# Kernel optimization log

Hardware: AMD Instinct MI355X
Metric: run time of the kernel (lower is better)

The kernel has to match this reference:

```python
import jax, jax.numpy as jnp
import numpy as np

B, V, L = 128, 128000, 200


def setup_inputs() -> dict:
    key = jax.random.key(0)
    k1, k2, k3, k4, k5, k6, k7 = jax.random.split(key, 7)
    return {
        "logits": jax.random.normal(k1, (B, V), dtype=jnp.float32),
        "presence_penalties": jax.random.uniform(k2, (B,), dtype=jnp.float32, minval=0.0, maxval=2.0),
        "frequency_penalties": jax.random.uniform(k3, (B,), dtype=jnp.float32, minval=0.0, maxval=2.0),
        "temperatures": jax.random.uniform(k4, (B,), dtype=jnp.float32, minval=0.5, maxval=1.5),
        "top_ps": jax.random.uniform(k5, (B,), dtype=jnp.float32, minval=0.7, maxval=1.0),
        "output_tokens": jax.random.randint(k6, (B, L), 0, V),
        "top_ks": jax.random.randint(k7, (B,), 1, 1000),
    }


def reference(logits, presence_penalties, frequency_penalties, temperatures,
              top_ps, output_tokens, top_ks):
    b, v = logits.shape
    # --- penalties: batched bincount via scatter-add (matches _batched_bincount,
    # including counting the 0-padded history tokens, as the torch code does) ---
    rows = jnp.arange(b)[:, None]
    occ = jnp.zeros((b, v), dtype=logits.dtype).at[rows, output_tokens].add(1.0)
    logits = logits - occ * frequency_penalties[:, None] \
                    - (occ > 0).astype(logits.dtype) * presence_penalties[:, None]
    # --- temperature ---
    logits = logits / temperatures[:, None]
    # --- top-p / top-k filtering (sort descending, mask, unsort) ---
    idx = jnp.argsort(-logits, axis=-1)                       # [b, v] descending order
    logits_sort = jnp.take_along_axis(logits, idx, axis=-1)
    probs_sort = jax.nn.softmax(logits_sort, axis=-1)
    probs_cum = jnp.cumsum(probs_sort, axis=-1)
    top_p_mask = (probs_cum - probs_sort) > top_ps[:, None]
    top_k_mask = jnp.arange(v)[None, :] >= top_ks[:, None]
    logits_sort = jnp.where(top_p_mask | top_k_mask, -jnp.inf, logits_sort)
    inv = jnp.argsort(idx, axis=-1)
    logits = jnp.take_along_axis(logits_sort, inv, axis=-1)   # back to vocab order
    # --- probs / logprobs ---
    probs = jax.nn.softmax(logits, axis=-1)
    logprobs = jax.nn.log_softmax(logits, axis=-1)
    # --- multinomial sample via Gumbel-max (deterministic fixed key) ---
    g = jax.random.gumbel(jax.random.key(42), (b, v), dtype=logits.dtype)
    next_tokens = jnp.argmax(logprobs + g, axis=-1)
    return probs, logprobs, next_tokens
```

## Files before the change

### kernel.cpp

```cpp
#include <hip/hip_runtime.h>
#include <stdint.h>


#define B_ 128
#define V_ 128000
#define L_ 200
#define NPREP_ 4
#define PQ_ (V_ / NPREP_)
#define PQ4_ (PQ_ / 4)
#define NCHUNK_ 16
#define CHUNK_ (V_ / NCHUNK_)
#define CHUNK4_ (CHUNK_ / 4)
#define NBIN_ 8192
#define PCAP_ 2048
#define CCAP_ (NPREP_ * PCAP_)
#define TCAP_ 2048

#define OFF_CAND_ 32
#define OFF_TIDX_ 50000
#define OFF_TYV_ 51000
#define OFF_HCNT_ 65568
static_assert(OFF_CAND_ + NPREP_ * 2 * PCAP_ <= OFF_TIDX_, "layout");
static_assert(OFF_TIDX_ + NPREP_ * L_ <= OFF_TYV_, "layout");
static_assert(OFF_TYV_ + NPREP_ * L_ <= OFF_HCNT_, "layout");
static_assert(OFF_HCNT_ + NPREP_ * NBIN_ <= V_, "layout");
static_assert(816 + L_ < CHUNK_, "relay layout");

#define JAX_PARTITIONABLE 1

__device__ __forceinline__ uint32_t f2key(float f) {
  uint32_t u = __float_as_uint(f);
  return (u & 0x80000000u) ? ~u : (u | 0x80000000u);
}
__device__ __forceinline__ float key2f(uint32_t k) {
  uint32_t u = (k & 0x80000000u) ? (k ^ 0x80000000u) : ~k;
  return __uint_as_float(u);
}
__device__ __forceinline__ float binhi(uint32_t bin) {
  return key2f((bin << 19) | 0x7FFFFu);
}

__device__ __forceinline__ float adj_pen(float x, float cnt, float fp, float pp, float tt) {
#pragma clang fp contract(off)
  return ((x - cnt * fp) - pp) / tt;
}
__device__ __forceinline__ float adj_plain(float x, float tt) {
#pragma clang fp contract(off)
  return x / tt;
}
__device__ __forceinline__ float fsub(float a, float b) {
#pragma clang fp contract(off)
  return a - b;
}

__device__ __forceinline__ void tf_round(uint32_t &a, uint32_t &b, int r) {
  a += b;
  b = (b << r) | (b >> (32 - r));
  b ^= a;
}
__device__ __forceinline__ void threefry2x32(uint32_t x0, uint32_t x1, uint32_t &o0, uint32_t &o1) {
  const uint32_t k0 = 0u, k1 = 42u;
  const uint32_t k2 = k0 ^ k1 ^ 0x1BD11BDAu;
  x0 += k0; x1 += k1;
  tf_round(x0, x1, 13); tf_round(x0, x1, 15); tf_round(x0, x1, 26); tf_round(x0, x1, 6);
  x0 += k1; x1 += k2 + 1u;
  tf_round(x0, x1, 17); tf_round(x0, x1, 29); tf_round(x0, x1, 16); tf_round(x0, x1, 24);
  x0 += k2; x1 += k0 + 2u;
  tf_round(x0, x1, 13); tf_round(x0, x1, 15); tf_round(x0, x1, 26); tf_round(x0, x1, 6);
  x0 += k0; x1 += k1 + 3u;
  tf_round(x0, x1, 17); tf_round(x0, x1, 29); tf_round(x0, x1, 16); tf_round(x0, x1, 24);
  x0 += k1; x1 += k2 + 4u;
  tf_round(x0, x1, 13); tf_round(x0, x1, 15); tf_round(x0, x1, 26); tf_round(x0, x1, 6);
  x0 += k2; x1 += k0 + 5u;
  o0 = x0; o1 = x1;
}
__device__ __forceinline__ float gumbel_at(uint32_t j) {
  uint32_t o0, o1, bits;
#if JAX_PARTITIONABLE
  threefry2x32(0u, j, o0, o1);
  bits = o0 ^ o1;
#else
  const uint32_t half = (uint32_t)B_ * (uint32_t)V_ / 2u;
  if (j < half) { threefry2x32(j, j + half, o0, o1); bits = o0; }
  else          { threefry2x32(j - half, j, o0, o1); bits = o1; }
#endif
  float u = __uint_as_float((bits >> 9) | 0x3f800000u) - 1.0f;
  float r = (u == 0.0f) ? 1.17549435e-38f : u;
  return -logf(-logf(r));
}

__global__ void __launch_bounds__(1024) k_prep_v14(
    const float* __restrict__ logits, const float* __restrict__ pres,
    const float* __restrict__ freq, const float* __restrict__ temps,
    const int* __restrict__ toks, float* __restrict__ probs) {
  const int b = blockIdx.y, q = blockIdx.x, tid = threadIdx.x;
  __shared__ int stok[L_];
  __shared__ uint32_t lhist[NBIN_];
  __shared__ uint32_t lk[PCAP_];
  __shared__ uint32_t li[PCAP_];
  __shared__ uint32_t bmap[PQ_ / 32];
  __shared__ uint32_t ptok[L_];
  __shared__ uint32_t pyv[L_];
  __shared__ uint32_t s_lcnt, s_pcnt;
  if (tid < L_) stok[tid] = toks[b * L_ + tid];
  for (int i = tid; i < NBIN_; i += 1024) lhist[i] = 0u;
  if (tid < PQ_ / 32 - 0) {  bmap[tid < PQ_ / 32 ? tid : 0] = 0u; }
  if (tid == 0) { s_lcnt = 0u; s_pcnt = 0u; }
  const float tt = temps[b];
  const uint32_t kth = f2key(adj_plain(2.0f, tt));
  __syncthreads();
  const int base4 = q * PQ4_;
  const int lo = q * PQ_;
  const float4* src = (const float4*)(logits + (size_t)b * V_);
  for (int it = 0; it < 8; ++it) {
    const int i4 = it * 1024 + tid;
    if (i4 < PQ4_) {
      const float4 x = src[base4 + i4];
      const float vv[4] = {adj_plain(x.x, tt), adj_plain(x.y, tt),
                           adj_plain(x.z, tt), adj_plain(x.w, tt)};
      const int v0 = (base4 + i4) * 4;
#pragma unroll
      for (int p = 0; p < 4; ++p) {
        const uint32_t k = f2key(vv[p]);
        atomicAdd(&lhist[k >> 19], 1u);
        if (k >= kth) {
          const uint32_t slot = atomicAdd(&s_lcnt, 1u);
          if (slot < PCAP_) { lk[slot] = k; li[slot] = (uint32_t)(v0 + p); }
        }
      }
    }
  }
  __syncthreads();
  if (tid < L_) {
    const int t0 = stok[tid];
    if (t0 >= lo && t0 < lo + PQ_) {
      int cnt = 0; bool first = true;
      for (int i = 0; i < L_; ++i) {
        const int ti = stok[i];
        cnt += (ti == t0);
        if (i < tid && ti == t0) first = false;
      }
      if (first) {
        const float x = logits[(size_t)b * V_ + t0];
        const float y_old = adj_plain(x, tt);
        const float y_new = adj_pen(x, (float)cnt, freq[b], pres[b], tt);
        atomicSub(&lhist[f2key(y_old) >> 19], 1u);
        atomicAdd(&lhist[f2key(y_new) >> 19], 1u);
        const int off = t0 - lo;
        atomicOr(&bmap[off >> 5], 1u << (off & 31));
        const uint32_t slot = atomicAdd(&s_pcnt, 1u);
        if (slot < (uint32_t)L_) {
          ptok[slot] = (uint32_t)t0;
          pyv[slot] = __float_as_uint(y_new);
        }
      }
    }
  }
  __syncthreads();
  const uint32_t lcnt = s_lcnt < PCAP_ ? s_lcnt : PCAP_;
  for (uint32_t i = tid; i < lcnt; i += 1024) {
    const uint32_t idx = li[i];
    const int off = (int)idx - lo;
    if (bmap[off >> 5] & (1u << (off & 31))) {
      int cnt = 0;
      for (int j = 0; j < L_; ++j) cnt += (stok[j] == (int)idx);
      const float x = logits[(size_t)b * V_ + idx];
      lk[i] = f2key(adj_pen(x, (float)cnt, freq[b], pres[b], tt));
    }
  }
  __syncthreads();
  uint32_t* stats = (uint32_t*)(probs + (size_t)b * V_);
  const uint32_t pcnt = s_pcnt < (uint32_t)L_ ? s_pcnt : (uint32_t)L_;
  if (tid == 0) {
    stats[1 + q] = lcnt;
    stats[16 + q] = pcnt;
  }
  uint32_t* slice = stats + OFF_HCNT_ + q * NBIN_;
  for (int i = tid; i < NBIN_; i += 1024) slice[i] = lhist[i];
  uint32_t* seg = stats + OFF_CAND_ + q * 2 * PCAP_;
  for (uint32_t i = tid; i < lcnt; i += 1024) {
    seg[2 * i] = lk[i]; seg[2 * i + 1] = li[i];
  }
  uint32_t* tidx = stats + OFF_TIDX_ + q * L_;
  uint32_t* tyv = stats + OFF_TYV_ + q * L_;
  for (uint32_t i = tid; i < pcnt; i += 1024) {
    tidx[i] = ptok[i]; tyv[i] = pyv[i];
  }
}

__global__ void __launch_bounds__(1024) k_mid_v14(
    const int* __restrict__ topks, const float* __restrict__ topps,
    float* __restrict__ probs, float* __restrict__ tail) {
  const int b = blockIdx.x, tid = threadIdx.x;
  uint32_t* stats = (uint32_t*)(probs + (size_t)b * V_);
  __shared__ uint32_t hcnt[NBIN_];
  __shared__ uint32_t sk[CCAP_];
  __shared__ uint32_t si[CCAP_];
  __shared__ uint32_t tbi[L_];
  __shared__ uint32_t tby[L_];
  __shared__ uint32_t tlist[TCAP_];
  __shared__ uint32_t ccnt[256];
  __shared__ float cw[256];
  __shared__ float zcw[256];
  __shared__ uint32_t mb[256];
  __shared__ uint32_t lh[256];
  __shared__ float scm[256];
  __shared__ uint32_t scc[256];
  __shared__ uint32_t sS[256];
  __shared__ float rf[1024];
  __shared__ unsigned long long ru[1024];
  __shared__ uint32_t s_r, s_prefix, s_pmask, s_tieE, s_tiemax, s_tcnt, s_n;
  __shared__ int s_pick, s_pick2, s_found;
  __shared__ float s_m;
  if (tid == 0) { s_tiemax = 0x7FFFFFFFu; s_tcnt = 0u; }
  const uint32_t c0 = stats[1] < PCAP_ ? stats[1] : PCAP_;
  const uint32_t c1 = stats[2] < PCAP_ ? stats[2] : PCAP_;
  const uint32_t c2 = stats[3] < PCAP_ ? stats[3] : PCAP_;
  const uint32_t c3 = stats[4] < PCAP_ ? stats[4] : PCAP_;
  const uint32_t e1 = c0 + c1, e2 = c0 + c1 + c2;
  const uint32_t C = e2 + c3;
  for (uint32_t c = tid; c < C; c += 1024) {
    uint32_t qq, rr;
    if (c < c0)      { qq = 0; rr = c; }
    else if (c < e1) { qq = 1; rr = c - c0; }
    else if (c < e2) { qq = 2; rr = c - e1; }
    else             { qq = 3; rr = c - e2; }
    const uint2 e = ((const uint2*)(stats + OFF_CAND_ + qq * 2 * PCAP_))[rr];
    sk[c] = e.x; si[c] = e.y;
  }
  uint32_t pc[NPREP_];
#pragma unroll
  for (int qq = 0; qq < NPREP_; ++qq) {
    const uint32_t nq = stats[16 + qq];
    pc[qq] = nq < (uint32_t)L_ ? nq : (uint32_t)L_;
  }
  uint32_t tp = 0;
#pragma unroll
  for (int qq = 0; qq < NPREP_; ++qq) {
    const uint32_t* gi = stats + OFF_TIDX_ + qq * L_;
    const uint32_t* gy = stats + OFF_TYV_ + qq * L_;
    for (uint32_t i = tid; i < pc[qq]; i += 1024) {
      const uint32_t d = tp + i;
      if (d < (uint32_t)L_) { tbi[d] = gi[i]; tby[d] = gy[i]; }
    }
    tp += pc[qq];
  }
  const uint32_t T = tp < (uint32_t)L_ ? tp : (uint32_t)L_;
  const uint32_t* hs = stats + OFF_HCNT_;
  for (int i = tid; i < NBIN_; i += 1024)
    hcnt[i] = hs[i] + hs[NBIN_ + i] + hs[2 * NBIN_ + i] + hs[3 * NBIN_ + i];
  __syncthreads();
  if (tid < 256) {
    uint32_t sc = 0; float sw = 0.0f; uint32_t mymb = 0u;
    const int hi = (NBIN_ - 1) - 32 * tid;
    for (int i = 0; i < 32; ++i) {
      const int bin = hi - i;
      const uint32_t c = hcnt[bin];
      sc += c;
      if (c) {
        sw += (float)c * __expf(binhi((uint32_t)bin));
        if ((uint32_t)bin > mymb) mymb = (uint32_t)bin;
      }
    }
    ccnt[tid] = sc; cw[tid] = sw; zcw[tid] = sw; mb[tid] = mymb;
  }
  __syncthreads();
  for (int s = 128; s > 0; s >>= 1) {
    if (tid < s) {
      mb[tid] = mb[tid] > mb[tid + s] ? mb[tid] : mb[tid + s];
      zcw[tid] += zcw[tid + s];
    }
    __syncthreads();
  }
  if (tid == 0) s_m = binhi(mb[0]);
  const float Z = zcw[0];
  const float limit = topps[b] * Z;
  if (tid < 256) { scm[tid] = cw[tid]; scc[tid] = ccnt[tid]; }
  __syncthreads();
  for (int off = 1; off < 256; off <<= 1) {
    float a = 0.0f; uint32_t u = 0u;
    const bool act = (tid < 256 && tid >= off);
    if (act) { a = scm[tid - off]; u = scc[tid - off]; }
    __syncthreads();
    if (act) { scm[tid] += a; scc[tid] += u; }
    __syncthreads();
  }
  if (tid == 0) s_pick = 256;
  __syncthreads();
  if (tid < 256) {
    const float ecm = tid ? scm[tid - 1] : 0.0f;
    if (ecm + cw[tid] > limit) atomicMin(&s_pick, tid);
  }
  __syncthreads();
  if (tid == 0) {
    uint32_t np = (uint32_t)V_;
    const int k = s_pick;
    if (k < 256) {
      float cm = k ? scm[k - 1] : 0.0f;
      uint32_t cc = k ? scc[k - 1] : 0u;
      const int hh = (NBIN_ - 1) - 32 * k;
      for (int i = 0; i < 32; ++i) {
        const int bin = hh - i;
        const uint32_t c = hcnt[bin];
        float rm = 0.0f;
        if (c) rm = (float)c * __expf(binhi((uint32_t)bin));
        cc += c; cm += rm;
        if (cm > limit) { np = cc; break; }
      }
    }
    const uint32_t K = (uint32_t)topks[b];
    uint32_t n = K < np ? K : np;
    if (n < 1u) n = 1u;
    s_n = n;
  }
  __syncthreads();
  const uint32_t n = s_n;
  if (tid == 0) s_pick2 = 256;
  __syncthreads();
  if (tid < 256) {
    if (scc[tid] >= n) atomicMin(&s_pick2, tid);
  }
  __syncthreads();
  if (tid == 0) {
    const int k2 = s_pick2 < 256 ? s_pick2 : 255;
    uint32_t cc = k2 ? scc[k2 - 1] : 0u;
    uint32_t istar = 0, cab = 0;
    const int hh = (NBIN_ - 1) - 32 * k2;
    for (int i = 0; i < 32; ++i) {
      const int bin = hh - i;
      if (cc + hcnt[bin] >= n) { istar = (uint32_t)bin; cab = cc; break; }
      cc += hcnt[bin];
    }
    s_r = n - cab;
    s_prefix = istar << 19;
    s_pmask = 0xFFF80000u;
  }
  __syncthreads();
  const float m = s_m;
  const int shifts[3] = {11, 3, 0};
  const uint32_t widths[3] = {256u, 256u, 8u};
  for (int p = 0; p < 3; ++p) {
    const int sh = shifts[p];
    const uint32_t w = widths[p];
    for (uint32_t i = tid; i < w; i += 1024) lh[i] = 0u;
    __syncthreads();
    const uint32_t pr = s_prefix, pm = s_pmask;
    for (uint32_t c = tid; c < C; c += 1024) {
      const uint32_t k = sk[c];
      if ((k & pm) == pr) atomicAdd(&lh[(k >> sh) & (w - 1u)], 1u);
    }
    __syncthreads();
    if (tid < (int)w) sS[tid] = lh[tid];
    __syncthreads();
    for (uint32_t off = 1; off < w; off <<= 1) {
      uint32_t a = 0u;
      const bool act = (tid + off < w);
      if (act) a = sS[tid + off];
      __syncthreads();
      if (act) sS[tid] += a;
      __syncthreads();
    }
    if (tid == 0) s_found = -1;
    __syncthreads();
    const uint32_t rr = s_r;
    if (tid < (int)w) {
      const uint32_t Shere = sS[tid];
      const uint32_t Snext = (tid + 1 < (int)w) ? sS[tid + 1] : 0u;
      if (Shere >= rr && Snext < rr) s_found = tid;
    }
    __syncthreads();
    if (tid == 0) {
      int found = s_found;
      if (found < 0) { found = 0; s_r = 1u; }
      else {
        const uint32_t Snext = (found + 1 < (int)w) ? sS[found + 1] : 0u;
        s_r = rr - Snext;
      }
      s_prefix = s_prefix | ((uint32_t)found << sh);
      s_pmask = s_pmask | ((w - 1u) << sh);
      s_tieE = lh[found];
    }
    __syncthreads();
  }
  const uint32_t tkey = s_prefix;
  const uint32_t ekeep = s_r;
  const uint32_t E = s_tieE;
  __syncthreads();
  if (ekeep < E && E <= (uint32_t)TCAP_) {
    for (uint32_t c = tid; c < C; c += 1024) {
      if (sk[c] == tkey) {
        const uint32_t pos = atomicAdd(&s_tcnt, 1u);
        if (pos < (uint32_t)TCAP_) tlist[pos] = si[c];
      }
    }
    __syncthreads();
    const uint32_t tc = s_tcnt < (uint32_t)TCAP_ ? s_tcnt : (uint32_t)TCAP_;
    for (uint32_t i = tid; i < tc; i += 1024) {
      const uint32_t mine = tlist[i];
      uint32_t rank = 0;
      for (uint32_t j = 0; j < tc; ++j) rank += (tlist[j] < mine) ? 1u : 0u;
      if (rank == ekeep - 1u) s_tiemax = mine;
    }
    __syncthreads();
  }
  const uint32_t tiemax = s_tiemax;
  float zp = 0.0f;
  for (uint32_t c = tid; c < C; c += 1024) {
    const uint32_t k = sk[c];
    if (k > tkey || (k == tkey && si[c] <= tiemax)) zp += expf(fsub(key2f(k), m));
  }
  rf[tid] = zp;
  __syncthreads();
  for (int s = 512; s > 0; s >>= 1) { if (tid < s) rf[tid] += rf[tid + s]; __syncthreads(); }
  const float Zp = rf[0];
  const float logZp = logf(Zp);
  unsigned long long best = 0ull;
  for (uint32_t c = tid; c < C; c += 1024) {
    const uint32_t k = sk[c];
    const uint32_t idx = si[c];
    if (k > tkey || (k == tkey && idx <= tiemax)) {
      const float lp = fsub(fsub(key2f(k), m), logZp);
      const float g = gumbel_at((uint32_t)b * (uint32_t)V_ + idx);
      const float sv = lp + g;
      const unsigned long long pk =
          ((unsigned long long)f2key(sv) << 32) | (unsigned long long)(~idx);
      if (pk > best) best = pk;
    }
  }
  ru[tid] = best;
  __syncthreads();
  for (int s = 512; s > 0; s >>= 1) {
    if (tid < s) ru[tid] = ru[tid] > ru[tid + s] ? ru[tid] : ru[tid + s];
    __syncthreads();
  }
  if (tid == 0) {
    const uint32_t bi = ~((uint32_t)(ru[0] & 0xFFFFFFFFull));
    tail[b] = (float)bi;
  }
  __syncthreads();
  if (tid < NCHUNK_) {
    uint32_t* cp = (uint32_t*)(probs + (size_t)b * V_ + (size_t)tid * CHUNK_);
    cp[0] = __float_as_uint(m);
    cp[1] = tkey;
    cp[2] = tiemax;
    cp[3] = __float_as_uint(Zp);
    cp[4] = __float_as_uint(logZp);
    cp[5] = T;
  }
  for (uint32_t i = tid; i < T; i += 1024) {
    const uint32_t a = tbi[i], yv = tby[i];
#pragma unroll
    for (int cc = 0; cc < NCHUNK_; ++cc) {
      uint32_t* cp = (uint32_t*)(probs + (size_t)b * V_ + (size_t)cc * CHUNK_);
      cp[16 + i] = a;
      cp[816 + i] = yv;
    }
  }
}

__global__ void __launch_bounds__(256) k_final_v14(
    const float* __restrict__ logits, const float* __restrict__ temps,
    float* __restrict__ probs, float* __restrict__ Ylp) {
  const int b = blockIdx.y, c = blockIdx.x, tid = threadIdx.x;
  float* cp = probs + (size_t)b * V_ + (size_t)c * CHUNK_;
  const uint32_t* cpu = (const uint32_t*)cp;
  __shared__ uint32_t sstat[6];
  __shared__ uint32_t tbi[L_], tby[L_];
  if (tid < 6) sstat[tid] = cpu[tid];
  __syncthreads();
  const uint32_t T = sstat[5] < (uint32_t)L_ ? sstat[5] : (uint32_t)L_;
  for (uint32_t i = tid; i < T; i += 256) { tbi[i] = cpu[16 + i]; tby[i] = cpu[816 + i]; }
  __syncthreads();
  const float m = __uint_as_float(sstat[0]);
  const uint32_t tkey = sstat[1];
  const uint32_t tiemax = sstat[2];
  const float Zp = __uint_as_float(sstat[3]);
  const float logZp = __uint_as_float(sstat[4]);
  const float tt = temps[b];
  const float nbig = -1e38f;
  const float4* xsrc = (const float4*)(logits + (size_t)b * V_ + (size_t)c * CHUNK_);
  float4* pdst = (float4*)cp;
  float4* ldst = (float4*)(Ylp + (size_t)b * V_ + (size_t)c * CHUNK_);
  for (int it = 0; it < 8; ++it) {
    const int i4 = it * 256 + tid;
    if (i4 < CHUNK4_) {
      const float4 x = xsrc[i4];
      const int v0 = c * CHUNK_ + i4 * 4;
      const float xx[4] = {x.x, x.y, x.z, x.w};
      float py[4], ly[4];
#pragma unroll
      for (int p = 0; p < 4; ++p) {
        const float yy = adj_plain(xx[p], tt);
        const uint32_t ky = f2key(yy);
        const bool kept = (ky > tkey) || (ky == tkey && (uint32_t)(v0 + p) <= tiemax);
        const float d = fsub(yy, m);
        py[p] = kept ? (expf(d) / Zp) : 0.0f;
        ly[p] = kept ? fsub(d, logZp) : nbig;
      }
      float4 p4; p4.x = py[0]; p4.y = py[1]; p4.z = py[2]; p4.w = py[3];
      float4 l4; l4.x = ly[0]; l4.y = ly[1]; l4.z = ly[2]; l4.w = ly[3];
      pdst[i4] = p4;
      ldst[i4] = l4;
    }
  }
  __syncthreads();
  const uint32_t clo = (uint32_t)(c * CHUNK_);
  for (uint32_t i = tid; i < T; i += 256) {
    const uint32_t idx = tbi[i];
    if (idx - clo < (uint32_t)CHUNK_) {
      const float y = __uint_as_float(tby[i]);
      const uint32_t ky = f2key(y);
      const bool kept = (ky > tkey) || (ky == tkey && idx <= tiemax);
      const float d = fsub(y, m);
      probs[(size_t)b * V_ + idx] = kept ? (expf(d) / Zp) : 0.0f;
      Ylp[(size_t)b * V_ + idx] = kept ? fsub(d, logZp) : nbig;
    }
  }
}

extern "C" void kernel_launch(void* const* d_in, const int* in_sizes, int n_in,
                              void* d_out, int out_size, void* d_ws, size_t ws_size,
                              hipStream_t stream) {
  (void)in_sizes; (void)n_in; (void)out_size; (void)d_ws; (void)ws_size;
  const float* logits = (const float*)d_in[0];
  const float* pres   = (const float*)d_in[1];
  const float* freq   = (const float*)d_in[2];
  const float* temps  = (const float*)d_in[3];
  const float* topps  = (const float*)d_in[4];
  const int*   toks   = (const int*)d_in[5];
  const int*   topks  = (const int*)d_in[6];
  float* probs = (float*)d_out;
  float* Ylp   = probs + (size_t)B_ * V_;
  float* tail  = probs + 2 * (size_t)B_ * V_;

  k_prep_v14 <<<dim3(NPREP_, B_),  dim3(1024), 0, stream>>>(logits, pres, freq, temps, toks, probs);
  k_mid_v14  <<<dim3(B_),          dim3(1024), 0, stream>>>(topks, topps, probs, tail);
  k_final_v14<<<dim3(NCHUNK_, B_), dim3(256),  0, stream>>>(logits, temps, probs, Ylp);
}
```

Measured before the change: 242.2 us.

## Fuse prep and mid kernels using last-block-done atomic counter per row

Merges the per-row selection stage into the prep kernel. Each of the four prep blocks per row bumps a workspace counter after a threadfence, and the last block to arrive runs the mid-stage logic, reusing a union of shared memory. This removes one kernel launch and the grid-wide barrier between stages, so mid work can overlap with other rows' prep. In exchange it adds a memset of the counters, a larger shared-memory footprint per prep block that may lower occupancy, and a fallback path when no workspace is provided.

Measured after the change: 299.2 us. 23.5% more time.

```diff
diff --git a/kernel.cpp b/kernel.cpp
--- a/kernel.cpp
+++ b/kernel.cpp
@@ -89,22 +89,53 @@
   return -logf(-logf(r));
 }
 
-__global__ void __launch_bounds__(1024) k_prep_v14(
+struct PrepS {
+  uint32_t lhist[NBIN_];
+  uint32_t lk[PCAP_];
+  uint32_t li[PCAP_];
+  uint32_t bmap[PQ_ / 32];
+  int stok[L_];
+  uint32_t ptok[L_];
+  uint32_t pyv[L_];
+};
+struct MidS {
+  uint32_t hcnt[NBIN_];
+  uint32_t sk[CCAP_];
+  uint32_t si[CCAP_];
+  uint32_t tlist[TCAP_];
+  uint32_t tbi[L_];
+  uint32_t tby[L_];
+  unsigned long long ru[1024];
+  float rf[1024];
+  uint32_t ccnt[256];
+  float cw[256];
+  float zcw[256];
+  uint32_t mb[256];
+  uint32_t lh[256];
+  float scm[256];
+  uint32_t scc[256];
+  uint32_t sS[256];
+};
+#define SMEM_BYTES_ (sizeof(MidS) > sizeof(PrepS) ? sizeof(MidS) : sizeof(PrepS))
+static_assert(SMEM_BYTES_ <= 150 * 1024, "LDS budget");
+
+__global__ void __launch_bounds__(1024) k_pm_v15(
     const float* __restrict__ logits, const float* __restrict__ pres,
     const float* __restrict__ freq, const float* __restrict__ temps,
-    const int* __restrict__ toks, float* __restrict__ probs) {
+    const float* __restrict__ topps, const int* __restrict__ toks,
+    const int* __restrict__ topks,
+    float* probs, float* __restrict__ tail, uint32_t* __restrict__ wscnt) {
   const int b = blockIdx.y, q = blockIdx.x, tid = threadIdx.x;
-  __shared__ int stok[L_];
-  __shared__ uint32_t lhist[NBIN_];
-  __shared__ uint32_t lk[PCAP_];
-  __shared__ uint32_t li[PCAP_];
-  __shared__ uint32_t bmap[PQ_ / 32];
-  __shared__ uint32_t ptok[L_];
-  __shared__ uint32_t pyv[L_];
-  __shared__ uint32_t s_lcnt, s_pcnt;
-  if (tid < L_) stok[tid] = toks[b * L_ + tid];
-  for (int i = tid; i < NBIN_; i += 1024) lhist[i] = 0u;
-  if (tid < PQ_ / 32 - 0) {  bmap[tid < PQ_ / 32 ? tid : 0] = 0u; }
+  __shared__ __align__(16) char smem_[SMEM_BYTES_];
+  PrepS* ps = (PrepS*)smem_;
+  __shared__ uint32_t s_lcnt, s_pcnt, s_last;
+  __shared__ uint32_t s_r, s_prefix, s_pmask, s_tieE, s_tiemax, s_tcnt, s_n;
+  __shared__ int s_pick, s_pick2, s_found;
+  __shared__ float s_m;
+
+  if (tid < L_) ps->stok[tid] = toks[b * L_ + tid];
+  for (int i = tid; i < NBIN_; i += 1024) ps->lhist[i] = 0u;
+  if (tid < PQ_ / 32) ps->bmap[tid] = 0u;
   if (tid == 0) { s_lcnt = 0u; s_pcnt = 0u; }
   const float tt = temps[b];
   const uint32_t kth = f2key(adj_plain(2.0f, tt));
@@ -122,21 +153,21 @@
 #pragma unroll
       for (int p = 0; p < 4; ++p) {
         const uint32_t k = f2key(vv[p]);
-        atomicAdd(&lhist[k >> 19], 1u);
+        atomicAdd(&ps->lhist[k >> 19], 1u);
         if (k >= kth) {
           const uint32_t slot = atomicAdd(&s_lcnt, 1u);
-          if (slot < PCAP_) { lk[slot] = k; li[slot] = (uint32_t)(v0 + p); }
+          if (slot < PCAP_) { ps->lk[slot] = k; ps->li[slot] = (uint32_t)(v0 + p); }
         }
       }
     }
   }
   __syncthreads();
   if (tid < L_) {
-    const int t0 = stok[tid];
+    const int t0 = ps->stok[tid];
     if (t0 >= lo && t0 < lo + PQ_) {
       int cnt = 0; bool first = true;
       for (int i = 0; i < L_; ++i) {
-        const int ti = stok[i];
+        const int ti = ps->stok[i];
         cnt += (ti == t0);
         if (i < tid && ti == t0) first = false;
       }
@@ -144,14 +175,14 @@
         const float x = logits[(size_t)b * V_ + t0];
         const float y_old = adj_plain(x, tt);
         const float y_new = adj_pen(x, (float)cnt, freq[b], pres[b], tt);
-        atomicSub(&lhist[f2key(y_old) >> 19], 1u);
-        atomicAdd(&lhist[f2key(y_new) >> 19], 1u);
+        atomicSub(&ps->lhist[f2key(y_old) >> 19], 1u);
+        atomicAdd(&ps->lhist[f2key(y_new) >> 19], 1u);
         const int off = t0 - lo;
-        atomicOr(&bmap[off >> 5], 1u << (off & 31));
+        atomicOr(&ps->bmap[off >> 5], 1u << (off & 31));
         const uint32_t slot = atomicAdd(&s_pcnt, 1u);
         if (slot < (uint32_t)L_) {
-          ptok[slot] = (uint32_t)t0;
-          pyv[slot] = __float_as_uint(y_new);
+          ps->ptok[slot] = (uint32_t)t0;
+          ps->pyv[slot] = __float_as_uint(y_new);
         }
       }
     }
@@ -159,13 +190,13 @@
   __syncthreads();
   const uint32_t lcnt = s_lcnt < PCAP_ ? s_lcnt : PCAP_;
   for (uint32_t i = tid; i < lcnt; i += 1024) {
-    const uint32_t idx = li[i];
+    const uint32_t idx = ps->li[i];
     const int off = (int)idx - lo;
-    if (bmap[off >> 5] & (1u << (off & 31))) {
+    if (ps->bmap[off >> 5] & (1u << (off & 31))) {
       int cnt = 0;
-      for (int j = 0; j < L_; ++j) cnt += (stok[j] == (int)idx);
+      for (int j = 0; j < L_; ++j) cnt += (ps->stok[j] == (int)idx);
       const float x = logits[(size_t)b * V_ + idx];
-      lk[i] = f2key(adj_pen(x, (float)cnt, freq[b], pres[b], tt));
+      ps->lk[i] = f2key(adj_pen(x, (float)cnt, freq[b], pres[b], tt));
     }
   }
   __syncthreads();
@@ -175,16 +206,274 @@
     stats[1 + q] = lcnt;
     stats[16 + q] = pcnt;
   }
-  uint32_t* slice = stats + OFF_HCNT_ + q * NBIN_;
-  for (int i = tid; i < NBIN_; i += 1024) slice[i] = lhist[i];
-  uint32_t* seg = stats + OFF_CAND_ + q * 2 * PCAP_;
-  for (uint32_t i = tid; i < lcnt; i += 1024) {
-    seg[2 * i] = lk[i]; seg[2 * i + 1] = li[i];
-  }
-  uint32_t* tidx = stats + OFF_TIDX_ + q * L_;
-  uint32_t* tyv = stats + OFF_TYV_ + q * L_;
-  for (uint32_t i = tid; i < pcnt; i += 1024) {
-    tidx[i] = ptok[i]; tyv[i] = pyv[i];
+  {
+    uint32_t* slice = stats + OFF_HCNT_ + q * NBIN_;
+    for (int i = tid; i < NBIN_; i += 1024) slice[i] = ps->lhist[i];
+    uint32_t* seg = stats + OFF_CAND_ + q * 2 * PCAP_;
+    for (uint32_t i = tid; i < lcnt; i += 1024) {
+      seg[2 * i] = ps->lk[i]; seg[2 * i + 1] = ps->li[i];
+    }
+    uint32_t* tidxp = stats + OFF_TIDX_ + q * L_;
+    uint32_t* tyvp = stats + OFF_TYV_ + q * L_;
+    for (uint32_t i = tid; i < pcnt; i += 1024) {
+      tidxp[i] = ps->ptok[i]; tyvp[i] = ps->pyv[i];
+    }
+  }
+  __syncthreads();
+  if (tid == 0) {
+    __threadfence();
+    const uint32_t old = atomicAdd(&wscnt[b], 1u);
+    s_last = (old == (uint32_t)(NPREP_ - 1)) ? 1u : 0u;
+  }
+  __syncthreads();
+  if (!s_last) return;
+  if (tid == 0) __threadfence();
+  __syncthreads();
+
+  MidS* md = (MidS*)smem_;
+  if (tid == 0) { s_tiemax = 0x7FFFFFFFu; s_tcnt = 0u; }
+  const uint32_t c0 = stats[1] < PCAP_ ? stats[1] : PCAP_;
+  const uint32_t c1 = stats[2] < PCAP_ ? stats[2] : PCAP_;
+  const uint32_t c2 = stats[3] < PCAP_ ? stats[3] : PCAP_;
+  const uint32_t c3 = stats[4] < PCAP_ ? stats[4] : PCAP_;
+  const uint32_t e1 = c0 + c1, e2 = c0 + c1 + c2;
+  const uint32_t C = e2 + c3;
+  for (uint32_t c = tid; c < C; c += 1024) {
+    uint32_t qq, rr;
+    if (c < c0)      { qq = 0; rr = c; }
+    else if (c < e1) { qq = 1; rr = c - c0; }
+    else if (c < e2) { qq = 2; rr = c - e1; }
+    else             { qq = 3; rr = c - e2; }
+    const uint2 e = ((const uint2*)(stats + OFF_CAND_ + qq * 2 * PCAP_))[rr];
+    md->sk[c] = e.x; md->si[c] = e.y;
+  }
+  uint32_t pc[NPREP_];
+#pragma unroll
+  for (int qq = 0; qq < NPREP_; ++qq) {
+    const uint32_t nq = stats[16 + qq];
+    pc[qq] = nq < (uint32_t)L_ ? nq : (uint32_t)L_;
+  }
+  uint32_t tp = 0;
+#pragma unroll
+  for (int qq = 0; qq < NPREP_; ++qq) {
+    const uint32_t* gi = stats + OFF_TIDX_ + qq * L_;
+    const uint32_t* gy = stats + OFF_TYV_ + qq * L_;
+    for (uint32_t i = tid; i < pc[qq]; i += 1024) {
+      const uint32_t d = tp + i;
+      if (d < (uint32_t)L_) { md->tbi[d] = gi[i]; md->tby[d] = gy[i]; }
+    }
+    tp += pc[qq];
+  }
+  const uint32_t T = tp < (uint32_t)L_ ? tp : (uint32_t)L_;
+  const uint32_t* hs = stats + OFF_HCNT_;
+  for (int i = tid; i < NBIN_; i += 1024)
+    md->hcnt[i] = hs[i] + hs[NBIN_ + i] + hs[2 * NBIN_ + i] + hs[3 * NBIN_ + i];
+  __syncthreads();
+  if (tid < 256) {
+    uint32_t sc = 0; float sw = 0.0f; uint32_t mymb = 0u;
+    const int hi = (NBIN_ - 1) - 32 * tid;
+    for (int i = 0; i < 32; ++i) {
+      const int bin = hi - i;
+      const uint32_t c = md->hcnt[bin];
+      sc += c;
+      if (c) {
+        sw += (float)c * __expf(binhi((uint32_t)bin));
+        if ((uint32_t)bin > mymb) mymb = (uint32_t)bin;
+      }
+    }
+    md->ccnt[tid] = sc; md->cw[tid] = sw; md->zcw[tid] = sw; md->mb[tid] = mymb;
+  }
+  __syncthreads();
+  for (int s = 128; s > 0; s >>= 1) {
+    if (tid < s) {
+      md->mb[tid] = md->mb[tid] > md->mb[tid + s] ? md->mb[tid] : md->mb[tid + s];
+      md->zcw[tid] += md->zcw[tid + s];
+    }
+    __syncthreads();
+  }
+  if (tid == 0) s_m = binhi(md->mb[0]);
+  const float Z = md->zcw[0];
+  const float limit = topps[b] * Z;
+  if (tid < 256) { md->scm[tid] = md->cw[tid]; md->scc[tid] = md->ccnt[tid]; }
+  __syncthreads();
+  for (int off = 1; off < 256; off <<= 1) {
+    float a = 0.0f; uint32_t u = 0u;
+    const bool act = (tid < 256 && tid >= off);
+    if (act) { a = md->scm[tid - off]; u = md->scc[tid - off]; }
+    __syncthreads();
+    if (act) { md->scm[tid] += a; md->scc[tid] += u; }
+    __syncthreads();
+  }
+  if (tid == 0) s_pick = 256;
+  __syncthreads();
+  if (tid < 256) {
+    const float ecm = tid ? md->scm[tid - 1] : 0.0f;
+    if (ecm + md->cw[tid] > limit) atomicMin(&s_pick, tid);
+  }
+  __syncthreads();
+  if (tid == 0) {
+    uint32_t np = (uint32_t)V_;
+    const int k = s_pick;
+    if (k < 256) {
+      float cm = k ? md->scm[k - 1] : 0.0f;
+      uint32_t cc = k ? md->scc[k - 1] : 0u;
+      const int hh = (NBIN_ - 1) - 32 * k;
+      for (int i = 0; i < 32; ++i) {
+        const int bin = hh - i;
+        const uint32_t c = md->hcnt[bin];
+        float rm = 0.0f;
+        if (c) rm = (float)c * __expf(binhi((uint32_t)bin));
+        cc += c; cm += rm;
+        if (cm > limit) { np = cc; break; }
+      }
+    }
+    const uint32_t K = (uint32_t)topks[b];
+    uint32_t n = K < np ? K : np;
+    if (n < 1u) n = 1u;
+    s_n = n;
+  }
+  __syncthreads();
+  const uint32_t n = s_n;
+  if (tid == 0) s_pick2 = 256;
+  __syncthreads();
+  if (tid < 256) {
+    if (md->scc[tid] >= n) atomicMin(&s_pick2, tid);
+  }
+  __syncthreads();
+  if (tid == 0) {
+    const int k2 = s_pick2 < 256 ? s_pick2 : 255;
+    uint32_t cc = k2 ? md->scc[k2 - 1] : 0u;
+    uint32_t istar = 0, cab = 0;
+    const int hh = (NBIN_ - 1) - 32 * k2;
+    for (int i = 0; i < 32; ++i) {
+      const int bin = hh - i;
+      if (cc + md->hcnt[bin] >= n) { istar = (uint32_t)bin; cab = cc; break; }
+      cc += md->hcnt[bin];
+    }
+    s_r = n - cab;
+    s_prefix = istar << 19;
+    s_pmask = 0xFFF80000u;
+  }
+  __syncthreads();
+  const float m = s_m;
+  const int shifts[3] = {11, 3, 0};
+  const uint32_t widths[3] = {256u, 256u, 8u};
+  for (int p = 0; p < 3; ++p) {
+    const int sh = shifts[p];
+    const uint32_t w = widths[p];
+    for (uint32_t i = tid; i < w; i += 1024) md->lh[i] = 0u;
+    __syncthreads();
+    const uint32_t pr = s_prefix, pm = s_pmask;
+    for (uint32_t c = tid; c < C; c += 1024) {
+      const uint32_t k = md->sk[c];
+      if ((k & pm) == pr) atomicAdd(&md->lh[(k >> sh) & (w - 1u)], 1u);
+    }
+    __syncthreads();
+    if (tid < (int)w) md->sS[tid] = md->lh[tid];
+    __syncthreads();
+    for (uint32_t off = 1; off < w; off <<= 1) {
+      uint32_t a = 0u;
+      const bool act = (tid + off < w);
+      if (act) a = md->sS[tid + off];
+      __syncthreads();
+      if (act) md->sS[tid] += a;
+      __syncthreads();
+    }
+    if (tid == 0) s_found = -1;
+    __syncthreads();
+    const uint32_t rr = s_r;
+    if (tid < (int)w) {
+      const uint32_t Shere = md->sS[tid];
+      const uint32_t Snext = (tid + 1 < (int)w) ? md->sS[tid + 1] : 0u;
+      if (Shere >= rr && Snext < rr) s_found = tid;
+    }
+    __syncthreads();
+    if (tid == 0) {
+      int found = s_found;
+      if (found < 0) { found = 0; s_r = 1u; }
+      else {
+        const uint32_t Snext = (found + 1 < (int)w) ? md->sS[found + 1] : 0u;
+        s_r = rr - Snext;
+      }
+      s_prefix = s_prefix | ((uint32_t)found << sh);
+      s_pmask = s_pmask | ((w - 1u) << sh);
+      s_tieE = md->lh[found];
+    }
+    __syncthreads();
+  }
+  const uint32_t tkey = s_prefix;
+  const uint32_t ekeep = s_r;
+  const uint32_t E = s_tieE;
+  __syncthreads();
+  if (ekeep < E && E <= (uint32_t)TCAP_) {
+    for (uint32_t c = tid; c < C; c += 1024) {
+      if (md->sk[c] == tkey) {
+        const uint32_t pos = atomicAdd(&s_tcnt, 1u);
+        if (pos < (uint32_t)TCAP_) md->tlist[pos] = md->si[c];
+      }
+    }
+    __syncthreads();
+    const uint32_t tc = s_tcnt < (uint32_t)TCAP_ ? s_tcnt : (uint32_t)TCAP_;
+    for (uint32_t i = tid; i < tc; i += 1024) {
+      const uint32_t mine = md->tlist[i];
+      uint32_t rank = 0;
+      for (uint32_t j = 0; j < tc; ++j) rank += (md->tlist[j] < mine) ? 1u : 0u;
+      if (rank == ekeep - 1u) s_tiemax = mine;
+    }
+    __syncthreads();
+  }
+  const uint32_t tiemax = s_tiemax;
+  float zp = 0.0f;
+  for (uint32_t c = tid; c < C; c += 1024) {
+    const uint32_t k = md->sk[c];
+    if (k > tkey || (k == tkey && md->si[c] <= tiemax)) zp += expf(fsub(key2f(k), m));
+  }
+  md->rf[tid] = zp;
+  __syncthreads();
+  for (int s = 512; s > 0; s >>= 1) { if (tid < s) md->rf[tid] += md->rf[tid + s]; __syncthreads(); }
+  const float Zp = md->rf[0];
+  const float logZp = logf(Zp);
+  unsigned long long best = 0ull;
+  for (uint32_t c = tid; c < C; c += 1024) {
+    const uint32_t k = md->sk[c];
+    const uint32_t idx = md->si[c];
+    if (k > tkey || (k == tkey && idx <= tiemax)) {
+      const float lp = fsub(fsub(key2f(k), m), logZp);
+      const float g = gumbel_at((uint32_t)b * (uint32_t)V_ + idx);
+      const float sv = lp + g;
+      const unsigned long long pk =
+          ((unsigned long long)f2key(sv) << 32) | (unsigned long long)(~idx);
+      if (pk > best) best = pk;
+    }
+  }
+  md->ru[tid] = best;
+  __syncthreads();
+  for (int s = 512; s > 0; s >>= 1) {
+    if (tid < s) md->ru[tid] = md->ru[tid] > md->ru[tid + s] ? md->ru[tid] : md->ru[tid + s];
+    __syncthreads();
+  }
+  if (tid == 0) {
+    const uint32_t bi = ~((uint32_t)(md->ru[0] & 0xFFFFFFFFull));
+    tail[b] = (float)bi;
+  }
+  __syncthreads();
+  if (tid < NCHUNK_) {
+    uint32_t* cp = (uint32_t*)(probs + (size_t)b * V_ + (size_t)tid * CHUNK_);
+    cp[0] = __float_as_uint(m);
+    cp[1] = tkey;
+    cp[2] = tiemax;
+    cp[3] = __float_as_uint(Zp);
+    cp[4] = __float_as_uint(logZp);
+    cp[5] = T;
+  }
+  for (uint32_t i = tid; i < T; i += 1024) {
+    const uint32_t a = md->tbi[i], yv = md->tby[i];
+#pragma unroll
+    for (int cc2 = 0; cc2 < NCHUNK_; ++cc2) {
+      uint32_t* cp = (uint32_t*)(probs + (size_t)b * V_ + (size_t)cc2 * CHUNK_);
+      cp[16 + i] = a;
+      cp[816 + i] = yv;
+    }
   }
 }
 
@@ -193,22 +482,8 @@
     float* __restrict__ probs, float* __restrict__ tail) {
   const int b = blockIdx.x, tid = threadIdx.x;
   uint32_t* stats = (uint32_t*)(probs + (size_t)b * V_);
-  __shared__ uint32_t hcnt[NBIN_];
-  __shared__ uint32_t sk[CCAP_];
-  __shared__ uint32_t si[CCAP_];
-  __shared__ uint32_t tbi[L_];
-  __shared__ uint32_t tby[L_];
-  __shared__ uint32_t tlist[TCAP_];
-  __shared__ uint32_t ccnt[256];
-  __shared__ float cw[256];
-  __shared__ float zcw[256];
-  __shared__ uint32_t mb[256];
-  __shared__ uint32_t lh[256];
-  __shared__ float scm[256];
-  __shared__ uint32_t scc[256];
-  __shared__ uint32_t sS[256];
-  __shared__ float rf[1024];
-  __shared__ unsigned long long ru[1024];
+  __shared__ __align__(16) char smem_[sizeof(MidS)];
+  MidS* md = (MidS*)smem_;
   __shared__ uint32_t s_r, s_prefix, s_pmask, s_tieE, s_tiemax, s_tcnt, s_n;
   __shared__ int s_pick, s_pick2, s_found;
   __shared__ float s_m;
@@ -226,7 +501,7 @@
     else if (c < e2) { qq = 2; rr = c - e1; }
     else             { qq = 3; rr = c - e2; }
     const uint2 e = ((const uint2*)(stats + OFF_CAND_ + qq * 2 * PCAP_))[rr];
-    sk[c] = e.x; si[c] = e.y;
+    md->sk[c] = e.x; md->si[c] = e.y;
   }
   uint32_t pc[NPREP_];
 #pragma unroll
@@ -241,67 +516,67 @@
     const uint32_t* gy = stats + OFF_TYV_ + qq * L_;
     for (uint32_t i = tid; i < pc[qq]; i += 1024) {
       const uint32_t d = tp + i;
-      if (d < (uint32_t)L_) { tbi[d] = gi[i]; tby[d] = gy[i]; }
+      if (d < (uint32_t)L_) { md->tbi[d] = gi[i]; md->tby[d] = gy[i]; }
     }
     tp += pc[qq];
   }
   const uint32_t T = tp < (uint32_t)L_ ? tp : (uint32_t)L_;
   const uint32_t* hs = stats + OFF_HCNT_;
   for (int i = tid; i < NBIN_; i += 1024)
-    hcnt[i] = hs[i] + hs[NBIN_ + i] + hs[2 * NBIN_ + i] + hs[3 * NBIN_ + i];
+    md->hcnt[i] = hs[i] + hs[NBIN_ + i] + hs[2 * NBIN_ + i] + hs[3 * NBIN_ + i];
   __syncthreads();
   if (tid < 256) {
     uint32_t sc = 0; float sw = 0.0f; uint32_t mymb = 0u;
     const int hi = (NBIN_ - 1) - 32 * tid;
     for (int i = 0; i < 32; ++i) {
       const int bin = hi - i;
-      const uint32_t c = hcnt[bin];
+      const uint32_t c = md->hcnt[bin];
       sc += c;
       if (c) {
         sw += (float)c * __expf(binhi((uint32_t)bin));
         if ((uint32_t)bin > mymb) mymb = (uint32_t)bin;
       }
     }
-    ccnt[tid] = sc; cw[tid] = sw; zcw[tid] = sw; mb[tid] = mymb;
+    md->ccnt[tid] = sc; md->cw[tid] = sw; md->zcw[tid] = sw; md->mb[tid] = mymb;
   }
   __syncthreads();
   for (int s = 128; s > 0; s >>= 1) {
     if (tid < s) {
-      mb[tid] = mb[tid] > mb[tid + s] ? mb[tid] : mb[tid + s];
-      zcw[tid] += zcw[tid + s];
-    }
-    __syncthreads();
-  }
-  if (tid == 0) s_m = binhi(mb[0]);
-  const float Z = zcw[0];
+      md->mb[tid] = md->mb[tid] > md->mb[tid + s] ? md->mb[tid] : md->mb[tid + s];
+      md->zcw[tid] += md->zcw[tid + s];
+    }
+    __syncthreads();
+  }
+  if (tid == 0) s_m = binhi(md->mb[0]);
+  const float Z = md->zcw[0];
   const float limit = topps[b] * Z;
-  if (tid < 256) { scm[tid] = cw[tid]; scc[tid] = ccnt[tid]; }
+  if (tid < 256) { md->scm[tid] = md->cw[tid]; md->scc[tid] = md->ccnt[tid]; }
   __syncthreads();
   for (int off = 1; off < 256; off <<= 1) {
     float a = 0.0f; uint32_t u = 0u;
     const bool act = (tid < 256 && tid >= off);
-    if (act) { a = scm[tid - off]; u = scc[tid - off]; }
-    __syncthreads();
-    if (act) { scm[tid] += a; scc[tid] += u; }
+    if (act) { a = md->scm[tid - off]; u = md->scc[tid - off]; }
+    __syncthreads();
+    if (act) { md->scm[tid] += a; md->scc[tid] += u; }
     __syncthreads();
   }
   if (tid == 0) s_pick = 256;
   __syncthreads();
   if (tid < 256) {
-    const float ecm = tid ? scm[tid - 1] : 0.0f;
-    if (ecm + cw[tid] > limit) atomicMin(&s_pick, tid);
+    const float ecm = tid ? md->scm[tid - 1] : 0.0f;
+    if (ecm + md->cw[tid] > limit) atomicMin(&s_pick, tid);
   }
   __syncthreads();
   if (tid == 0) {
     uint32_t np = (uint32_t)V_;
     const int k = s_pick;
     if (k < 256) {
-      float cm = k ? scm[k - 1] : 0.0f;
-      uint32_t cc = k ? scc[k - 1] : 0u;
+      float cm = k ? md->scm[k - 1] : 0.0f;
+      uint32_t cc = k ? md->scc[k - 1] : 0u;
       const int hh = (NBIN_ - 1) - 32 * k;
       for (int i = 0; i < 32; ++i) {
         const int bin = hh - i;
-        const uint32_t c = hcnt[bin];
+        const uint32_t c = md->hcnt[bin];
         float rm = 0.0f;
         if (c) rm = (float)c * __expf(binhi((uint32_t)bin));
         cc += c; cm += rm;
@@ -318,18 +593,18 @@
   if (tid == 0) s_pick2 = 256;
   __syncthreads();
   if (tid < 256) {
-    if (scc[tid] >= n) atomicMin(&s_pick2, tid);
+    if (md->scc[tid] >= n) atomicMin(&s_pick2, tid);
   }
   __syncthreads();
   if (tid == 0) {
     const int k2 = s_pick2 < 256 ? s_pick2 : 255;
-    uint32_t cc = k2 ? scc[k2 - 1] : 0u;
+    uint32_t cc = k2 ? md->scc[k2 - 1] : 0u;
     uint32_t istar = 0, cab = 0;
     const int hh = (NBIN_ - 1) - 32 * k2;
     for (int i = 0; i < 32; ++i) {
       const int bin = hh - i;
-      if (cc + hcnt[bin] >= n) { istar = (uint32_t)bin; cab = cc; break; }
-      cc += hcnt[bin];
+      if (cc + md->hcnt[bin] >= n) { istar = (uint32_t)bin; cab = cc; break; }
+      cc += md->hcnt[bin];
     }
     s_r = n - cab;
     s_prefix = istar << 19;
@@ -342,30 +617,30 @@
   for (int p = 0; p < 3; ++p) {
     const int sh = shifts[p];
     const uint32_t w = widths[p];
-    for (uint32_t i = tid; i < w; i += 1024) lh[i] = 0u;
+    for (uint32_t i = tid; i < w; i += 1024) md->lh[i] = 0u;
     __syncthreads();
     const uint32_t pr = s_prefix, pm = s_pmask;
     for (uint32_t c = tid; c < C; c += 1024) {
-      const uint32_t k = sk[c];
-      if ((k & pm) == pr) atomicAdd(&lh[(k >> sh) & (w - 1u)], 1u);
-    }
-    __syncthreads();
-    if (tid < (int)w) sS[tid] = lh[tid];
+      const uint32_t k = md->sk[c];
+      if ((k & pm) == pr) atomicAdd(&md->lh[(k >> sh) & (w - 1u)], 1u);
+    }
+    __syncthreads();
+    if (tid < (int)w) md->sS[tid] = md->lh[tid];
     __syncthreads();
     for (uint32_t off = 1; off < w; off <<= 1) {
       uint32_t a = 0u;
       const bool act = (tid + off < w);
-      if (act) a = sS[tid + off];
+      if (act) a = md->sS[tid + off];
       __syncthreads();
-      if (act) sS[tid] += a;
+      if (act) md->sS[tid] += a;
       __syncthreads();
     }
     if (tid == 0) s_found = -1;
     __syncthreads();
     const uint32_t rr = s_r;
     if (tid < (int)w) {
-      const uint32_t Shere = sS[tid];
-      const uint32_t Snext = (tid + 1 < (int)w) ? sS[tid + 1] : 0u;
+      const uint32_t Shere = md->sS[tid];
+      const uint32_t Snext = (tid + 1 < (int)w) ? md->sS[tid + 1] : 0u;
       if (Shere >= rr && Snext < rr) s_found = tid;
     }
     __syncthreads();
@@ -373,12 +648,12 @@
       int found = s_found;
       if (found < 0) { found = 0; s_r = 1u; }
       else {
-        const uint32_t Snext = (found + 1 < (int)w) ? sS[found + 1] : 0u;
+        const uint32_t Snext = (found + 1 < (int)w) ? md->sS[found + 1] : 0u;
         s_r = rr - Snext;
       }
       s_prefix = s_prefix | ((uint32_t)found << sh);
       s_pmask = s_pmask | ((w - 1u) << sh);
-      s_tieE = lh[found];
+      s_tieE = md->lh[found];
     }
     __syncthreads();
   }
@@ -388,17 +663,17 @@
   __syncthreads();
   if (ekeep < E && E <= (uint32_t)TCAP_) {
     for (uint32_t c = tid; c < C; c += 1024) {
-      if (sk[c] == tkey) {
+      if (md->sk[c] == tkey) {
         const uint32_t pos = atomicAdd(&s_tcnt, 1u);
-        if (pos < (uint32_t)TCAP_) tlist[pos] = si[c];
+        if (pos < (uint32_t)TCAP_) md->tlist[pos] = md->si[c];
       }
     }
     __syncthreads();
     const uint32_t tc = s_tcnt < (uint32_t)TCAP_ ? s_tcnt : (uint32_t)TCAP_;
     for (uint32_t i = tid; i < tc; i += 1024) {
-      const uint32_t mine = tlist[i];
+      const uint32_t mine = md->tlist[i];
       uint32_t rank = 0;
-      for (uint32_t j = 0; j < tc; ++j) rank += (tlist[j] < mine) ? 1u : 0u;
+      for (uint32_t j = 0; j < tc; ++j) rank += (md->tlist[j] < mine) ? 1u : 0u;
       if (rank == ekeep - 1u) s_tiemax = mine;
     }
     __syncthreads();
@@ -406,18 +681,18 @@
   const uint32_t tiemax = s_tiemax;
   float zp = 0.0f;
   for (uint32_t c = tid; c < C; c += 1024) {
-    const uint32_t k = sk[c];
-    if (k > tkey || (k == tkey && si[c] <= tiemax)) zp += expf(fsub(key2f(k), m));
-  }
-  rf[tid] = zp;
-  __syncthreads();
-  for (int s = 512; s > 0; s >>= 1) { if (tid < s) rf[tid] += rf[tid + s]; __syncthreads(); }
-  const float Zp = rf[0];
+    const uint32_t k = md->sk[c];
+    if (k > tkey || (k == tkey && md->si[c] <= tiemax)) zp += expf(fsub(key2f(k), m));
+  }
+  md->rf[tid] = zp;
+  __syncthreads();
+  for (int s = 512; s > 0; s >>= 1) { if (tid < s) md->rf[tid] += md->rf[tid + s]; __syncthreads(); }
+  const float Zp = md->rf[0];
   const float logZp = logf(Zp);
   unsigned long long best = 0ull;
   for (uint32_t c = tid; c < C; c += 1024) {
-    const uint32_t k = sk[c];
-    const uint32_t idx = si[c];
+    const uint32_t k = md->sk[c];
+    const uint32_t idx = md->si[c];
     if (k > tkey || (k == tkey && idx <= tiemax)) {
       const float lp = fsub(fsub(key2f(k), m), logZp);
       const float g = gumbel_at((uint32_t)b * (uint32_t)V_ + idx);
@@ -427,14 +702,14 @@
       if (pk > best) best = pk;
     }
   }
-  ru[tid] = best;
+  md->ru[tid] = best;
   __syncthreads();
   for (int s = 512; s > 0; s >>= 1) {
-    if (tid < s) ru[tid] = ru[tid] > ru[tid + s] ? ru[tid] : ru[tid + s];
+    if (tid < s) md->ru[tid] = md->ru[tid] > md->ru[tid + s] ? md->ru[tid] : md->ru[tid + s];
     __syncthreads();
   }
   if (tid == 0) {
-    const uint32_t bi = ~((uint32_t)(ru[0] & 0xFFFFFFFFull));
+    const uint32_t bi = ~((uint32_t)(md->ru[0] & 0xFFFFFFFFull));
     tail[b] = (float)bi;
   }
   __syncthreads();
@@ -448,13 +723,107 @@
     cp[5] = T;
   }
   for (uint32_t i = tid; i < T; i += 1024) {
-    const uint32_t a = tbi[i], yv = tby[i];
+    const uint32_t a = md->tbi[i], yv = md->tby[i];
 #pragma unroll
-    for (int cc = 0; cc < NCHUNK_; ++cc) {
-      uint32_t* cp = (uint32_t*)(probs + (size_t)b * V_ + (size_t)cc * CHUNK_);
+    for (int cc2 = 0; cc2 < NCHUNK_; ++cc2) {
+      uint32_t* cp = (uint32_t*)(probs + (size_t)b * V_ + (size_t)cc2 * CHUNK_);
       cp[16 + i] = a;
       cp[816 + i] = yv;
     }
+  }
+}
+
+__global__ void __launch_bounds__(1024) k_prep_v14(
+    const float* __restrict__ logits, const float* __restrict__ pres,
+    const float* __restrict__ freq, const float* __restrict__ temps,
+    const int* __restrict__ toks, float* __restrict__ probs) {
+  const int b = blockIdx.y, q = blockIdx.x, tid = threadIdx.x;
+  __shared__ __align__(16) char smem_[sizeof(PrepS)];
+  PrepS* ps = (PrepS*)smem_;
+  __shared__ uint32_t s_lcnt, s_pcnt;
+  if (tid < L_) ps->stok[tid] = toks[b * L_ + tid];
+  for (int i = tid; i < NBIN_; i += 1024) ps->lhist[i] = 0u;
+  if (tid < PQ_ / 32) ps->bmap[tid] = 0u;
+  if (tid == 0) { s_lcnt = 0u; s_pcnt = 0u; }
+  const float tt = temps[b];
+  const uint32_t kth = f2key(adj_plain(2.0f, tt));
+  __syncthreads();
+  const int base4 = q * PQ4_;
+  const int lo = q * PQ_;
+  const float4* src = (const float4*)(logits + (size_t)b * V_);
+  for (int it = 0; it < 8; ++it) {
+    const int i4 = it * 1024 + tid;
+    if (i4 < PQ4_) {
+      const float4 x = src[base4 + i4];
+      const float vv[4] = {adj_plain(x.x, tt), adj_plain(x.y, tt),
+                           adj_plain(x.z, tt), adj_plain(x.w, tt)};
+      const int v0 = (base4 + i4) * 4;
+#pragma unroll
+      for (int p = 0; p < 4; ++p) {
+        const uint32_t k = f2key(vv[p]);
+        atomicAdd(&ps->lhist[k >> 19], 1u);
+        if (k >= kth) {
+          const uint32_t slot = atomicAdd(&s_lcnt, 1u);
+          if (slot < PCAP_) { ps->lk[slot] = k; ps->li[slot] = (uint32_t)(v0 + p); }
+        }
+      }
+    }
+  }
+  __syncthreads();
+  if (tid < L_) {
+    const int t0 = ps->stok[tid];
+    if (t0 >= lo && t0 < lo + PQ_) {
+      int cnt = 0; bool first = true;
+      for (int i = 0; i < L_; ++i) {
+        const int ti = ps->stok[i];
+        cnt += (ti == t0);
+        if (i < tid && ti == t0) first = false;
+      }
+      if (first) {
+        const float x = logits[(size_t)b * V_ + t0];
+        const float y_old = adj_plain(x, tt);
+        const float y_new = adj_pen(x, (float)cnt, freq[b], pres[b], tt);
+        atomicSub(&ps->lhist[f2key(y_old) >> 19], 1u);
+        atomicAdd(&ps->lhist[f2key(y_new) >> 19], 1u);
+        const int off = t0 - lo;
+        atomicOr(&ps->bmap[off >> 5], 1u << (off & 31));
+        const uint32_t slot = atomicAdd(&s_pcnt, 1u);
+        if (slot < (uint32_t)L_) {
+          ps->ptok[slot] = (uint32_t)t0;
+          ps->pyv[slot] = __float_as_uint(y_new);
+        }
+      }
+    }
+  }
+  __syncthreads();
+  const uint32_t lcnt = s_lcnt < PCAP_ ? s_lcnt : PCAP_;
+  for (uint32_t i = tid; i < lcnt; i += 1024) {
+    const uint32_t idx = ps->li[i];
+    const int off = (int)idx - lo;
+    if (ps->bmap[off >> 5] & (1u << (off & 31))) {
+      int cnt = 0;
+      for (int j = 0; j < L_; ++j) cnt += (ps->stok[j] == (int)idx);
+      const float x = logits[(size_t)b * V_ + idx];
+      ps->lk[i] = f2key(adj_pen(x, (float)cnt, freq[b], pres[b], tt));
+    }
+  }
+  __syncthreads();
+  uint32_t* stats = (uint32_t*)(probs + (size_t)b * V_);
+  const uint32_t pcnt = s_pcnt < (uint32_t)L_ ? s_pcnt : (uint32_t)L_;
+  if (tid == 0) {
+    stats[1 + q] = lcnt;
+    stats[16 + q] = pcnt;
+  }
+  uint32_t* slice = stats + OFF_HCNT_ + q * NBIN_;
+  for (int i = tid; i < NBIN_; i += 1024) slice[i] = ps->lhist[i];
+  uint32_t* seg = stats + OFF_CAND_ + q * 2 * PCAP_;
+  for (uint32_t i = tid; i < lcnt; i += 1024) {
+    seg[2 * i] = ps->lk[i]; seg[2 * i + 1] = ps->li[i];
+  }
+  uint32_t* tidxp = stats + OFF_TIDX_ + q * L_;
+  uint32_t* tyvp = stats + OFF_TYV_ + q * L_;
+  for (uint32_t i = tid; i < pcnt; i += 1024) {
+    tidxp[i] = ps->ptok[i]; tyvp[i] = ps->pyv[i];
   }
 }
 
@@ -521,7 +890,7 @@
 extern "C" void kernel_launch(void* const* d_in, const int* in_sizes, int n_in,
                               void* d_out, int out_size, void* d_ws, size_t ws_size,
                               hipStream_t stream) {
-  (void)in_sizes; (void)n_in; (void)out_size; (void)d_ws; (void)ws_size;
+  (void)in_sizes; (void)n_in; (void)out_size;
   const float* logits = (const float*)d_in[0];
   const float* pres   = (const float*)d_in[1];
   const float* freq   = (const float*)d_in[2];
@@ -533,6 +902,17 @@
   float* Ylp   = probs + (size_t)B_ * V_;
   float* tail  = probs + 2 * (size_t)B_ * V_;
 
+  if (d_ws != nullptr && ws_size >= (size_t)(B_ * 4)) {
+    hipError_t em = hipMemsetAsync(d_ws, 0, (size_t)(B_ * 4), stream);
+    if (em == hipSuccess) {
+      k_pm_v15<<<dim3(NPREP_, B_), dim3(1024), 0, stream>>>(
+          logits, pres, freq, temps, topps, toks, topks, probs, tail,
+          (uint32_t*)d_ws);
+      k_final_v14<<<dim3(NCHUNK_, B_), dim3(256), 0, stream>>>(logits, temps, probs, Ylp);
+      return;
+    }
+    (void)hipGetLastError();
+  }
   k_prep_v14 <<<dim3(NPREP_, B_),  dim3(1024), 0, stream>>>(logits, pres, freq, temps, toks, probs);
   k_mid_v14  <<<dim3(B_),          dim3(1024), 0, stream>>>(topks, topps, probs, tail);
   k_final_v14<<<dim3(NCHUNK_, B_), dim3(256),  0, stream>>>(logits, temps, probs, Ylp);
```
